# Kernel optimization log

Hardware: AMD Instinct MI355X
Metric: run time of the kernel (lower is better)

Reference implementation:

```python
import jax, jax.numpy as jnp
import numpy as np

WINDOW = 128
BACKWARD = 1
FORWARD = 0

def look_around(x, pad_value):
    # x: [b, windows, window_size, ...]; pad window axis and gather shifted windows
    w = x.shape[1]
    pads = [(0, 0), (BACKWARD, FORWARD)] + [(0, 0)] * (x.ndim - 2)
    p = jnp.pad(x, pads, constant_values=pad_value)
    return jnp.concatenate([p[:, i:i + w] for i in range(BACKWARD + FORWARD + 1)], axis=2)

def setup_inputs() -> dict:
    key = jax.random.key(0)
    ks = jax.random.split(key, 5)
    shp = (2, 16, 4096, 64)
    names = ['q', 'k', 'q_rot', 'k_rot', 'v']
    inp = {n: jax.random.normal(ks[i], shp, dtype=jnp.float32) for i, n in enumerate(names)}
    inp['states'] = 0
    inp['inferring_states'] = 0
    return inp

def reference(q, k, q_rot, k_rot, v, states, inferring_states):
    shape = q.shape
    merge = lambda t: t.reshape(-1, t.shape[-2], t.shape[-1])
    q, k, q_rot, k_rot, v = map(merge, (q, k, q_rot, k_rot, v))
    b, t, e = q.shape
    windows = t // WINDOW
    ticker = jnp.arange(t, dtype=q.dtype)[None, :]
    b_t = ticker.reshape(1, windows, WINDOW)
    bucket = lambda x: x.reshape(b, windows, WINDOW, e)
    bq, bk, bq_rot, bk_rot, bv = map(bucket, (q, k, q_rot, k_rot, v))
    bk = look_around(bk, 0.0)
    bk_rot = look_around(bk_rot, 0.0)
    bv = look_around(bv, 0.0)
    bq_t = b_t
    bq_k = look_around(b_t, -1.0)
    scale = e ** (-0.5)
    dots = jnp.einsum('bwie,bwje->bwij', bq, bk) * scale
    dots_rot = jnp.einsum('bwie,bwje->bwij', bq_rot, bk_rot) * scale
    mask_value = -jnp.finfo(dots.dtype).max
    causal_mask = bq_t[:, :, :, None] < bq_k[:, :, None, :]
    pad_mask = bq_k[:, :, None, :] == -1
    mask = causal_mask | pad_mask
    dots = jnp.where(mask, mask_value, dots)
    dots_rot = jnp.where(mask, mask_value, dots_rot)
    attn = jax.nn.softmax(dots + dots_rot, axis=-1)
    out = jnp.einsum('bwij,bwje->bwie', attn, bv)
    return out.reshape(shape)
```

## Files before the change

kernel.cpp:

```cpp
#include <hip/hip_runtime.h>
#include <stdint.h>

#define T 4096
#define E 64
#define NWIN 32
#define NBH 32
#define KK_LD 136
#define VT_LD 136
#define PB_LD 144
#define PB_STRIDE (16*PB_LD)
#define VT_BYTES (64*VT_LD*2)
#define SMEM_BYTES (VT_BYTES + 8*PB_STRIDE*2)

typedef __attribute__((ext_vector_type(8))) short short8;
typedef __attribute__((ext_vector_type(4))) short short4v;
typedef __attribute__((ext_vector_type(4))) float f32x4;

__device__ __forceinline__ short f2bf(float x) {
  unsigned u = __float_as_uint(x);
  u += 0x7fffu + ((u >> 16) & 1u);
  return (short)(u >> 16);
}

__global__ __launch_bounds__(512, 4)
void la_kernel(const float* __restrict__ qg, const float* __restrict__ kg,
               const float* __restrict__ qrg, const float* __restrict__ krg,
               const float* __restrict__ vg, float* __restrict__ outg) {
  extern __shared__ char smem[];
  short* KK = (short*)smem;
  short* Vt = (short*)smem;
  short* Pb = (short*)(smem + VT_BYTES);

  const int w   = blockIdx.x;
  const int bh  = blockIdx.y;
  const int tid = threadIdx.x;
  const int wid  = tid >> 6;
  const int lane = tid & 63;
  const int li = lane & 15;
  const int lg = lane >> 4;

  const size_t base = (size_t)bh * T * E;
  const int krow0 = w * 128 - 128;
  const int rowb = wid * 16 + lg * 4;

  const int qrow = w * 128 + wid * 16 + li;
  const float* qp  = qg  + base + (size_t)qrow * E;
  const float* qrp = qrg + base + (size_t)qrow * E;
  short8 aF[4];
#pragma unroll
  for (int kt = 0; kt < 4; ++kt) {
    const float* sp = (kt < 2 ? qp : qrp) + (kt & 1) * 32 + lg * 8;
    float4 f0 = *(const float4*)sp;
    float4 f1 = *(const float4*)(sp + 4);
    short8 a;
    a[0]=f2bf(f0.x*0.125f); a[1]=f2bf(f0.y*0.125f); a[2]=f2bf(f0.z*0.125f); a[3]=f2bf(f0.w*0.125f);
    a[4]=f2bf(f1.x*0.125f); a[5]=f2bf(f1.y*0.125f); a[6]=f2bf(f1.z*0.125f); a[7]=f2bf(f1.w*0.125f);
    aF[kt] = a;
  }

  f32x4 O[4] = {{0,0,0,0},{0,0,0,0},{0,0,0,0},{0,0,0,0}};
  float m_run[4] = {-1e30f, -1e30f, -1e30f, -1e30f};
  float l_run[4] = {0.f, 0.f, 0.f, 0.f};

#pragma unroll 1
  for (int c = 0; c < 2; ++c) {
    if (w == 0 && c == 0) continue;
    const int kbase = krow0 + c * 128;

#pragma unroll
    for (int m = 0; m < 2; ++m) {
      const float* src = m ? krg : kg;
#pragma unroll
      for (int it = 0; it < 4; ++it) {
        int idx = it * 512 + tid;
        int row = idx >> 4, c4 = idx & 15;
        float4 f = *(const float4*)(src + base + (size_t)(kbase + row) * E + c4 * 4);
        short4v h = { f2bf(f.x), f2bf(f.y), f2bf(f.z), f2bf(f.w) };
        *(short4v*)(KK + row * KK_LD + m * 64 + c4 * 4) = h;
      }
    }
    __syncthreads();

    f32x4 S[8];
#pragma unroll
    for (int ct = 0; ct < 8; ++ct) {
      f32x4 acc = {0.f, 0.f, 0.f, 0.f};
      const short* kb = KK + (ct * 16 + li) * KK_LD + lg * 8;
#pragma unroll
      for (int kt = 0; kt < 4; ++kt) {
        short8 b = *(const short8*)(kb + kt * 32);
        acc = __builtin_amdgcn_mfma_f32_16x16x32_bf16(aF[kt], b, acc, 0, 0, 0);
      }
      S[ct] = acc;
    }

    float alpha[4];
#pragma unroll
    for (int r = 0; r < 4; ++r) {
      const int qi = rowb + r;
      float mx = -1e30f;
#pragma unroll
      for (int ct = 0; ct < 8; ++ct) {
        if (c == 1) {
          int jj = ct * 16 + li;
          if (jj > qi) S[ct][r] = -1e30f;
        }
        mx = fmaxf(mx, S[ct][r]);
      }
      mx = fmaxf(mx, __shfl_xor(mx, 1));
      mx = fmaxf(mx, __shfl_xor(mx, 2));
      mx = fmaxf(mx, __shfl_xor(mx, 4));
      mx = fmaxf(mx, __shfl_xor(mx, 8));
      float m_new = fmaxf(m_run[r], mx);
      float al = __expf(m_run[r] - m_new);
      float sm = 0.f;
#pragma unroll
      for (int ct = 0; ct < 8; ++ct) {
        float e = __expf(S[ct][r] - m_new);
        S[ct][r] = e;
        sm += e;
      }
      sm += __shfl_xor(sm, 1);
      sm += __shfl_xor(sm, 2);
      sm += __shfl_xor(sm, 4);
      sm += __shfl_xor(sm, 8);
      l_run[r] = l_run[r] * al + sm;
      m_run[r] = m_new;
      alpha[r] = al;
    }
#pragma unroll
    for (int nt = 0; nt < 4; ++nt)
#pragma unroll
      for (int r = 0; r < 4; ++r)
        O[nt][r] *= alpha[r];

    __syncthreads();

    short* pw = Pb + wid * PB_STRIDE;
#pragma unroll
    for (int ct = 0; ct < 8; ++ct) {
#pragma unroll
      for (int r = 0; r < 4; ++r) {
        pw[(lg * 4 + r) * PB_LD + ct * 16 + li] = f2bf(S[ct][r]);
      }
    }
    {
      const float* vp = vg + base + (size_t)(kbase + wid * 16) * E + lane;
#pragma unroll
      for (int rq = 0; rq < 4; ++rq) {
        short4v h;
#pragma unroll
        for (int j = 0; j < 4; ++j) {
          h[j] = f2bf(vp[(size_t)(rq * 4 + j) * E]);
        }
        *(short4v*)(Vt + lane * VT_LD + wid * 16 + rq * 4) = h;
      }
    }
    __syncthreads();

    short8 aP[4];
    const short* pr = Pb + wid * PB_STRIDE + li * PB_LD + lg * 8;
#pragma unroll
    for (int kt = 0; kt < 4; ++kt) aP[kt] = *(const short8*)(pr + kt * 32);
#pragma unroll
    for (int kt = 0; kt < 4; ++kt) {
#pragma unroll
      for (int nt = 0; nt < 4; ++nt) {
        short8 b = *(const short8*)(Vt + (nt * 16 + li) * VT_LD + kt * 32 + lg * 8);
        O[nt] = __builtin_amdgcn_mfma_f32_16x16x32_bf16(aP[kt], b, O[nt], 0, 0, 0);
      }
    }
    __syncthreads();
  }

  float* op = outg + base + (size_t)(w * 128 + rowb) * E;
#pragma unroll
  for (int r = 0; r < 4; ++r) {
    float linv = 1.f / l_run[r];
#pragma unroll
    for (int nt = 0; nt < 4; ++nt) {
      op[(size_t)r * E + nt * 16 + li] = O[nt][r] * linv;
    }
  }
}

extern "C" void kernel_launch(void* const* d_in, const int* in_sizes, int n_in,
                              void* d_out, int out_size, void* d_ws, size_t ws_size,
                              hipStream_t stream) {
  const float* q  = (const float*)d_in[0];
  const float* k  = (const float*)d_in[1];
  const float* qr = (const float*)d_in[2];
  const float* kr = (const float*)d_in[3];
  const float* v  = (const float*)d_in[4];
  float* out = (float*)d_out;
  dim3 grid(NWIN, NBH);
  la_kernel<<<grid, dim3(512), SMEM_BYTES, stream>>>(q, k, qr, kr, v, out);
}
```

Measured before the change: 220.1 us.

## Precompute bf16 K/Krot and transposed V, DMA them into swizzled LDS

Adds two pre-pass kernels that convert K and K_rot to a fused bf16 [T,128] buffer and transpose V to bf16 [E,T] in workspace. The attention kernel then loads these tiles with global_load_lds DMA into XOR-swizzled shared memory rather than converting them per block, and reuses the K buffer for the P tile, dropping one barrier. Each K/V tile was previously converted twice, once by each neighbouring window, so this removes redundant conversion and per-element strided V loads. In exchange it adds extra kernel launches and a round trip through workspace memory.

```diff
diff --git a/kernel.cpp b/kernel.cpp
--- a/kernel.cpp
+++ b/kernel.cpp
@@ -5,15 +5,10 @@
 #define E 64
 #define NWIN 32
 #define NBH 32
-#define KK_LD 136
-#define VT_LD 136
-#define PB_LD 144
-#define PB_STRIDE (16*PB_LD)
-#define VT_BYTES (64*VT_LD*2)
-#define SMEM_BYTES (VT_BYTES + 8*PB_STRIDE*2)
+#define CH 128
+#define SMEM_BYTES 49152
 
 typedef __attribute__((ext_vector_type(8))) short short8;
-typedef __attribute__((ext_vector_type(4))) short short4v;
 typedef __attribute__((ext_vector_type(4))) float f32x4;
 
 __device__ __forceinline__ short f2bf(float x) {
@@ -22,30 +17,77 @@
   return (short)(u >> 16);
 }
 
+__device__ __forceinline__ void dma16(const void* g, void* l) {
+  __builtin_amdgcn_global_load_lds(
+      (const __attribute__((address_space(1))) unsigned int*)g,
+      (__attribute__((address_space(3))) unsigned int*)l, 16, 0, 0);
+}
+
+__global__ __launch_bounds__(256)
+void fuse_kk(const float* __restrict__ k, const float* __restrict__ kr,
+             short* __restrict__ kkb) {
+  int gid = blockIdx.x * 256 + threadIdx.x;
+  int row = gid >> 3;
+  int sub = gid & 7;
+  int col = sub * 16;
+  const float* src = (col < 64) ? (k + (size_t)row * 64 + col)
+                                : (kr + (size_t)row * 64 + (col - 64));
+  float4 f0 = ((const float4*)src)[0];
+  float4 f1 = ((const float4*)src)[1];
+  float4 f2 = ((const float4*)src)[2];
+  float4 f3 = ((const float4*)src)[3];
+  short8 h0, h1;
+  h0[0]=f2bf(f0.x); h0[1]=f2bf(f0.y); h0[2]=f2bf(f0.z); h0[3]=f2bf(f0.w);
+  h0[4]=f2bf(f1.x); h0[5]=f2bf(f1.y); h0[6]=f2bf(f1.z); h0[7]=f2bf(f1.w);
+  h1[0]=f2bf(f2.x); h1[1]=f2bf(f2.y); h1[2]=f2bf(f2.z); h1[3]=f2bf(f2.w);
+  h1[4]=f2bf(f3.x); h1[5]=f2bf(f3.y); h1[6]=f2bf(f3.z); h1[7]=f2bf(f3.w);
+  short8* dst = (short8*)(kkb + (size_t)row * CH + col);
+  dst[0] = h0; dst[1] = h1;
+}
+
+__global__ __launch_bounds__(256)
+void transpose_v(const float* __restrict__ v, short* __restrict__ vtb) {
+  __shared__ float tile[64][68];
+  const int t0 = blockIdx.x * 64;
+  const int bh = blockIdx.y;
+  const float* vp = v + ((size_t)bh * T + t0) * E;
+  const int r = threadIdx.x >> 4, c = threadIdx.x & 15;
+#pragma unroll
+  for (int i = 0; i < 4; ++i) {
+    float4 f = *(const float4*)(vp + (size_t)(r + 16 * i) * E + c * 4);
+    *(float4*)(&tile[r + 16 * i][c * 4]) = f;
+  }
+  __syncthreads();
+  const int e = threadIdx.x >> 2, c2 = threadIdx.x & 3;
+  short8 h0, h1;
+#pragma unroll
+  for (int j = 0; j < 8; ++j) h0[j] = f2bf(tile[c2 * 16 + j][e]);
+#pragma unroll
+  for (int j = 0; j < 8; ++j) h1[j] = f2bf(tile[c2 * 16 + 8 + j][e]);
+  short8* dst = (short8*)(vtb + ((size_t)bh * E + e) * T + t0 + c2 * 16);
+  dst[0] = h0; dst[1] = h1;
+}
+
 __global__ __launch_bounds__(512, 4)
-void la_kernel(const float* __restrict__ qg, const float* __restrict__ kg,
-               const float* __restrict__ qrg, const float* __restrict__ krg,
-               const float* __restrict__ vg, float* __restrict__ outg) {
+void la_attn(const float* __restrict__ qg, const float* __restrict__ qrg,
+             const short* __restrict__ kkb, const short* __restrict__ vtb,
+             float* __restrict__ outg) {
   extern __shared__ char smem[];
-  short* KK = (short*)smem;
-  short* Vt = (short*)smem;
-  short* Pb = (short*)(smem + VT_BYTES);
-
-  const int w   = blockIdx.x;
-  const int bh  = blockIdx.y;
+  short* KKs = (short*)smem;
+  short* Vts = (short*)(smem + 32768);
+
+  const int w = blockIdx.x, bh = blockIdx.y;
   const int tid = threadIdx.x;
-  const int wid  = tid >> 6;
-  const int lane = tid & 63;
-  const int li = lane & 15;
-  const int lg = lane >> 4;
-
-  const size_t base = (size_t)bh * T * E;
+  const int wid = tid >> 6, lane = tid & 63;
+  const int li = lane & 15, lg = lane >> 4;
+
+  const size_t qbase = (size_t)bh * T * E;
   const int krow0 = w * 128 - 128;
   const int rowb = wid * 16 + lg * 4;
 
   const int qrow = w * 128 + wid * 16 + li;
-  const float* qp  = qg  + base + (size_t)qrow * E;
-  const float* qrp = qrg + base + (size_t)qrow * E;
+  const float* qp  = qg  + qbase + (size_t)qrow * E;
+  const float* qrp = qrg + qbase + (size_t)qrow * E;
   short8 aF[4];
 #pragma unroll
   for (int kt = 0; kt < 4; ++kt) {
@@ -67,16 +109,24 @@
     if (w == 0 && c == 0) continue;
     const int kbase = krow0 + c * 128;
 
-#pragma unroll
-    for (int m = 0; m < 2; ++m) {
-      const float* src = m ? krg : kg;
-#pragma unroll
-      for (int it = 0; it < 4; ++it) {
-        int idx = it * 512 + tid;
-        int row = idx >> 4, c4 = idx & 15;
-        float4 f = *(const float4*)(src + base + (size_t)(kbase + row) * E + c4 * 4);
-        short4v h = { f2bf(f.x), f2bf(f.y), f2bf(f.z), f2bf(f.w) };
-        *(short4v*)(KK + row * KK_LD + m * 64 + c4 * 4) = h;
+    {
+      const int rl = lane >> 4;
+      const int cbl = lane & 15;
+      const short* kksrc = kkb + ((size_t)bh * T + kbase) * CH;
+#pragma unroll
+      for (int ii = 0; ii < 4; ++ii) {
+        int r0 = wid * 16 + ii * 4;
+        int row = r0 + rl;
+        int cbg = cbl ^ (row & 15);
+        dma16(kksrc + (size_t)row * CH + cbg * 8, KKs + r0 * CH);
+      }
+      const short* vsrc = vtb + (size_t)bh * E * T + kbase;
+#pragma unroll
+      for (int ii = 0; ii < 2; ++ii) {
+        int r0 = wid * 8 + ii * 4;
+        int e = r0 + rl;
+        int cbg = cbl ^ (e & 15);
+        dma16(vsrc + (size_t)e * T + cbg * 8, Vts + r0 * CH);
       }
     }
     __syncthreads();
@@ -85,14 +135,15 @@
 #pragma unroll
     for (int ct = 0; ct < 8; ++ct) {
       f32x4 acc = {0.f, 0.f, 0.f, 0.f};
-      const short* kb = KK + (ct * 16 + li) * KK_LD + lg * 8;
+      const short* kb = KKs + (ct * 16 + li) * CH;
 #pragma unroll
       for (int kt = 0; kt < 4; ++kt) {
-        short8 b = *(const short8*)(kb + kt * 32);
+        short8 b = *(const short8*)(kb + ((kt * 4 + lg) ^ li) * 8);
         acc = __builtin_amdgcn_mfma_f32_16x16x32_bf16(aF[kt], b, acc, 0, 0, 0);
       }
       S[ct] = acc;
     }
+    __syncthreads();
 
     float alpha[4];
 #pragma unroll
@@ -134,46 +185,33 @@
       for (int r = 0; r < 4; ++r)
         O[nt][r] *= alpha[r];
 
+    short* pw = KKs + wid * 16 * CH;
+#pragma unroll
+    for (int ct = 0; ct < 8; ++ct) {
+#pragma unroll
+      for (int r = 0; r < 4; ++r) {
+        int prow = lg * 4 + r;
+        int cbl = ((ct * 2 + (li >> 3)) ^ prow);
+        pw[prow * CH + cbl * 8 + (li & 7)] = f2bf(S[ct][r]);
+      }
+    }
+
+    short8 aP[4];
+#pragma unroll
+    for (int kt = 0; kt < 4; ++kt)
+      aP[kt] = *(const short8*)(pw + li * CH + ((kt * 4 + lg) ^ li) * 8);
+#pragma unroll
+    for (int kt = 0; kt < 4; ++kt) {
+#pragma unroll
+      for (int nt = 0; nt < 4; ++nt) {
+        short8 b = *(const short8*)(Vts + (nt * 16 + li) * CH + ((kt * 4 + lg) ^ li) * 8);
+        O[nt] = __builtin_amdgcn_mfma_f32_16x16x32_bf16(aP[kt], b, O[nt], 0, 0, 0);
+      }
+    }
     __syncthreads();
-
-    short* pw = Pb + wid * PB_STRIDE;
-#pragma unroll
-    for (int ct = 0; ct < 8; ++ct) {
-#pragma unroll
-      for (int r = 0; r < 4; ++r) {
-        pw[(lg * 4 + r) * PB_LD + ct * 16 + li] = f2bf(S[ct][r]);
-      }
-    }
-    {
-      const float* vp = vg + base + (size_t)(kbase + wid * 16) * E + lane;
-#pragma unroll
-      for (int rq = 0; rq < 4; ++rq) {
-        short4v h;
-#pragma unroll
-        for (int j = 0; j < 4; ++j) {
-          h[j] = f2bf(vp[(size_t)(rq * 4 + j) * E]);
-        }
-        *(short4v*)(Vt + lane * VT_LD + wid * 16 + rq * 4) = h;
-      }
-    }
-    __syncthreads();
-
-    short8 aP[4];
-    const short* pr = Pb + wid * PB_STRIDE + li * PB_LD + lg * 8;
-#pragma unroll
-    for (int kt = 0; kt < 4; ++kt) aP[kt] = *(const short8*)(pr + kt * 32);
-#pragma unroll
-    for (int kt = 0; kt < 4; ++kt) {
-#pragma unroll
-      for (int nt = 0; nt < 4; ++nt) {
-        short8 b = *(const short8*)(Vt + (nt * 16 + li) * VT_LD + kt * 32 + lg * 8);
-        O[nt] = __builtin_amdgcn_mfma_f32_16x16x32_bf16(aP[kt], b, O[nt], 0, 0, 0);
-      }
-    }
-    __syncthreads();
-  }
-
-  float* op = outg + base + (size_t)(w * 128 + rowb) * E;
+  }
+
+  float* op = outg + qbase + (size_t)(w * 128 + rowb) * E;
 #pragma unroll
   for (int r = 0; r < 4; ++r) {
     float linv = 1.f / l_run[r];
@@ -193,6 +231,11 @@
   const float* kr = (const float*)d_in[3];
   const float* v  = (const float*)d_in[4];
   float* out = (float*)d_out;
-  dim3 grid(NWIN, NBH);
-  la_kernel<<<grid, dim3(512), SMEM_BYTES, stream>>>(q, k, qr, kr, v, out);
-}
+
+  short* kkb = (short*)d_ws;
+  short* vtb = kkb + (size_t)NBH * T * CH;
+
+  fuse_kk<<<4096, 256, 0, stream>>>(k, kr, kkb);
+  transpose_v<<<dim3(64, 32), 256, 0, stream>>>(v, vtb);
+  la_attn<<<dim3(NWIN, NBH), 512, SMEM_BYTES, stream>>>(q, qr, kkb, vtb, out);
+}
```

Result: slower. 247.6 us (+12.5%).
